# Optimization experiments

Hardware: AMD Instinct MI355X
Metric: run time of the kernel (lower is better)

The kernel has to match this reference:

```python
import jax, jax.numpy as jnp
import numpy as np
from jax import lax

SAMPLE_RATE = 44100.0


def _biquad(x, b0, b1, b2, a1, a2):
    """Direct-form-I biquad over last axis. x: [B,C,S]; coefs: [B,1] (broadcast over C).
    y[n] = b0*x[n] + b1*x[n-1] + b2*x[n-2] - a1*y[n-1] - a2*y[n-2], zero initial state
    (identical to torchaudio.functional.biquad)."""

    def step(carry, xn):  # xn: [B,C]
        x1, x2, y1, y2 = carry
        y = b0 * xn + b1 * x1 + b2 * x2 - a1 * y1 - a2 * y2
        return (xn, x1, y, y1), y

    xs = jnp.moveaxis(x, -1, 0)  # [S,B,C]
    z = jnp.zeros_like(x[..., 0])
    _, ys = lax.scan(step, (z, z, z, z), xs)
    return jnp.moveaxis(ys, 0, -1)  # [B,C,S]


def _peaking_coeffs(freq, gain, q):
    """RBJ peaking EQ coefficients, normalized by a0. Inputs: [B] -> outputs [B,1]."""
    w0 = 2.0 * jnp.pi * freq / SAMPLE_RATE
    alpha = jnp.sin(w0) / (2.0 * q)
    A = jnp.power(10.0, gain / 40.0)
    cosw0 = jnp.cos(w0)
    b0 = 1.0 + alpha * A
    b1 = -2.0 * cosw0
    b2 = 1.0 - alpha * A
    a0 = 1.0 + alpha / A
    a1 = -2.0 * cosw0
    a2 = 1.0 - alpha / A
    coefs = (b0 / a0, b1 / a0, b2 / a0, a1 / a0, a2 / a0)
    return tuple(c[:, None] for c in coefs)  # broadcast over channel dim


def setup_inputs() -> dict:
    key = jax.random.key(0)
    k1, k2, k3, k4 = jax.random.split(key, 4)
    B, C, S, NB = 32, 2, 262144, 10
    audio = jax.random.normal(k1, (B, C, S), dtype=jnp.float32)
    center_freqs = jax.random.uniform(k2, (B, NB), dtype=jnp.float32, minval=100.0, maxval=10000.0)
    gains = jax.random.uniform(k3, (B, NB), dtype=jnp.float32, minval=-12.0, maxval=12.0)
    q_factors = jax.random.uniform(k4, (B, NB), dtype=jnp.float32, minval=0.5, maxval=4.0)
    return {"audio": audio, "center_freqs": center_freqs, "gains": gains, "q_factors": q_factors}


def reference(audio, center_freqs, gains, q_factors):
    num_bands = center_freqs.shape[1]
    out = audio
    for band in range(num_bands):  # fixed small cascade of structurally distinct filters
        b0, b1, b2, a1, a2 = _peaking_coeffs(center_freqs[:, band], gains[:, band], q_factors[:, band])
        out = _biquad(out, b0, b1, b2, a1, a2)
    return out
```

## Files before the change

### kernel.cpp

```cpp
#include <hip/hip_runtime.h>


#define B_   32
#define C_   2
#define S_   262144
#define NB   10
#define SEQ  64

#define F_LCH   64
#define F_PCH   4096
#define F_G     8
#define F_GRP   512
#define F_NPOW  11

#define F_OFF_POW 1600
#define F_OFF_T   142400
#define F_OFF_G   5385280
#define F_OFF_SB  6040640
#define F_TOT     6696000

__global__ __launch_bounds__(256) void setup_kernel(
    const float* __restrict__ freqs, const float* __restrict__ gains,
    const float* __restrict__ qs, float* __restrict__ coef,
    float* __restrict__ powers) {
  __shared__ float bufA[400], bufB[400];
  __shared__ float cfs[NB * 5];
  const int b = blockIdx.x, tid = threadIdx.x;
  for (int e = tid; e < 400; e += 256) bufA[e] = 0.0f;
  if (tid < NB) {
    int idx = b * NB + tid;
    float f = freqs[idx], g = gains[idx], Q = qs[idx];
    float w0 = 6.28318530717958648f * f / 44100.0f;
    float sw = sinf(w0), cw = cosf(w0);
    float alpha = sw / (2.0f * Q);
    float A = expf(g * 0.05756462732485114f);
    float aA = alpha * A, adA = alpha / A;
    float inv = 1.0f / (1.0f + adA);
    float c0 = (1.0f + aA) * inv;
    float c1 = -2.0f * cw * inv;
    float c2 = (1.0f - aA) * inv;
    float c3 = 2.0f * cw * inv;
    float c4 = -(1.0f - adA) * inv;
    cfs[tid*5+0] = c0; cfs[tid*5+1] = c1; cfs[tid*5+2] = c2;
    cfs[tid*5+3] = c3; cfs[tid*5+4] = c4;
    float* o = coef + idx * 5;
    o[0] = c0; o[1] = c1; o[2] = c2; o[3] = c3; o[4] = c4;
  }
  __syncthreads();
  if (tid < 20) {
    int c = tid;
    float rp = 0.0f;
    for (int k = 0; k < NB; k++) {
      float b0 = cfs[k*5+0], b1 = cfs[k*5+1], b2 = cfs[k*5+2];
      float na1 = cfs[k*5+3], na2 = cfs[k*5+4];
      float val = (k > 0) ? b0 * rp : 0.0f;
      if (k > 0) {
        if (c == 2*k-2) val += b1;
        if (c == 2*k-1) val += b2;
      }
      if (c == 2*k)   val += na1;
      if (c == 2*k+1) val += na2;
      bufA[2*k*20 + c] = val;
      rp = val;
      if (c == 2*k) bufA[(2*k+1)*20 + c] = 1.0f;
    }
  }
  __syncthreads();
  float* cur = bufA;
  float* nxt = bufB;
  float* pw = powers + (size_t)b * F_NPOW * 400;
  for (int j = 1; j <= 17; j++) {
    for (int e = tid; e < 400; e += 256) {
      int r = e / 20, c = e % 20;
      float acc = 0.0f;
      #pragma unroll
      for (int k = 0; k < 20; k++) acc = fmaf(cur[r*20+k], cur[k*20+c], acc);
      nxt[e] = acc;
    }
    __syncthreads();
    { float* t_ = cur; cur = nxt; nxt = t_; }
    int slot = -1;
    if (j == 6) slot = 0;
    else if (j == 8) slot = 1;
    else if (j == 9) slot = 2;
    else if (j >= 10) slot = j - 7;
    if (slot >= 0) for (int e = tid; e < 400; e += 256) pw[slot*400 + e] = cur[e];
  }
}

template <bool WRITE_OUT>
__global__ __launch_bounds__(64) void pass_v3(
    const float* __restrict__ x, const float* __restrict__ coef,
    const float* __restrict__ tst, float* __restrict__ tout,
    float* __restrict__ out) {
  __shared__ float4 lds4[1024];
  const int seq = blockIdx.y;
  const int b = seq >> 1;
  const int lane = threadIdx.x;
  const int wgc0 = blockIdx.x * 64;
  const int chunk = wgc0 + lane;
  const float* cf = coef + b * NB * 5;
  float b0[NB], b1[NB], b2[NB], na1[NB], na2[NB];
  #pragma unroll
  for (int k = 0; k < NB; k++) {
    b0[k] = cf[k*5+0]; b1[k] = cf[k*5+1]; b2[k] = cf[k*5+2];
    na1[k] = cf[k*5+3]; na2[k] = cf[k*5+4];
  }
  const size_t span0 = (size_t)seq * S_ + (size_t)wgc0 * F_LCH;
  const float4* gx = (const float4*)(x + span0);
  #pragma unroll 4
  for (int it = 0; it < 16; it++) {
    int f = it * 64 + lane;
    float4 v = gx[f];
    int c = f >> 4, q = f & 15;
    lds4[c*16 + (q ^ (c & 15))] = v;
  }
  __syncthreads();
  float x1 = 0.0f, x2 = 0.0f;
  if (lane == 0) {
    if (chunk > 0) {
      const float* xs = x + span0;
      x1 = xs[-1]; x2 = xs[-2];
    }
  } else {
    float4 pv = lds4[(lane-1)*16 + (15 ^ ((lane-1) & 15))];
    x2 = pv.z; x1 = pv.w;
  }
  float p[NB], q_[NB];
  if (WRITE_OUT && chunk > 0) {
    const float4* sv = (const float4*)(tst + ((size_t)seq * F_PCH + chunk - 1) * 20);
    #pragma unroll
    for (int i = 0; i < 5; i++) {
      float4 a = sv[i];
      p[2*i] = a.x; q_[2*i] = a.y; p[2*i+1] = a.z; q_[2*i+1] = a.w;
    }
  } else {
    #pragma unroll
    for (int k = 0; k < NB; k++) { p[k] = 0.0f; q_[k] = 0.0f; }
  }
  #pragma unroll 2
  for (int qq = 0; qq < 16; qq++) {
    const int slot = lane*16 + (qq ^ (lane & 15));
    float4 xv = lds4[slot];
    float xin[4] = {xv.x, xv.y, xv.z, xv.w};
    float o[4];
    #pragma unroll
    for (int j = 0; j < 4; j++) {
      float u = xin[j], u1 = x1, u2 = x2;
      x2 = x1; x1 = xin[j];
      #pragma unroll
      for (int k = 0; k < NB; k++) {
        float v = fmaf(b0[k], u,
                  fmaf(b1[k], u1,
                  fmaf(b2[k], u2,
                  fmaf(na1[k], p[k], na2[k] * q_[k]))));
        u1 = p[k]; u2 = q_[k];
        q_[k] = p[k]; p[k] = v;
        u = v;
      }
      o[j] = u;
    }
    if (WRITE_OUT) lds4[slot] = make_float4(o[0], o[1], o[2], o[3]);
  }
  if (WRITE_OUT) {
    __syncthreads();
    float4* gy = (float4*)(out + span0);
    #pragma unroll 4
    for (int it = 0; it < 16; it++) {
      int f = it * 64 + lane;
      int c = f >> 4, q = f & 15;
      gy[f] = lds4[c*16 + (q ^ (c & 15))];
    }
  } else {
    float4* td = (float4*)(tout + ((size_t)seq * F_PCH + chunk) * 20);
    #pragma unroll
    for (int i = 0; i < 5; i++)
      td[i] = make_float4(p[2*i], q_[2*i], p[2*i+1], q_[2*i+1]);
  }
}

template <bool WRITE_BACK>
__global__ __launch_bounds__(256) void scan_horner(
    float* __restrict__ t, const float* __restrict__ powers,
    float* __restrict__ gbuf, const float* __restrict__ sbuf) {
  __shared__ float Msh[400];
  const int seq = blockIdx.y, b = seq >> 1;
  const int g = blockIdx.x * 256 + threadIdx.x;
  const float* pw0 = powers + (size_t)b * F_NPOW * 400;
  for (int e = threadIdx.x; e < 400; e += 256) {
    int r = e / 20, c = e % 20;
    Msh[c*20 + r] = pw0[e];
  }
  __syncthreads();
  float s[20];
  if (WRITE_BACK) {
    const float4* sv = (const float4*)(sbuf + ((size_t)seq * F_GRP + g) * 20);
    #pragma unroll
    for (int i = 0; i < 5; i++) {
      float4 a = sv[i];
      s[4*i] = a.x; s[4*i+1] = a.y; s[4*i+2] = a.z; s[4*i+3] = a.w;
    }
  } else {
    #pragma unroll
    for (int r = 0; r < 20; r++) s[r] = 0.0f;
  }
  float* tp = t + ((size_t)seq * F_PCH + (size_t)g * F_G) * 20;
  const float4* tv = (const float4*)tp;
  float4 nx[5];
  #pragma unroll
  for (int i = 0; i < 5; i++) nx[i] = tv[i];
  #pragma unroll 1
  for (int j = 0; j < F_G; j++) {
    float ns[20];
    #pragma unroll
    for (int i = 0; i < 5; i++) {
      float4 a = nx[i];
      ns[4*i] = a.x; ns[4*i+1] = a.y; ns[4*i+2] = a.z; ns[4*i+3] = a.w;
    }
    if (j < F_G - 1) {
      #pragma unroll
      for (int i = 0; i < 5; i++) nx[i] = tv[(j+1)*5 + i];
    }
    #pragma unroll
    for (int c = 0; c < 20; c++) {
      float vc = s[c];
      const float4* col = (const float4*)&Msh[c*20];
      float4 c0 = col[0], c1 = col[1], c2 = col[2], c3 = col[3], c4 = col[4];
      ns[0]  = fmaf(c0.x, vc, ns[0]);  ns[1]  = fmaf(c0.y, vc, ns[1]);
      ns[2]  = fmaf(c0.z, vc, ns[2]);  ns[3]  = fmaf(c0.w, vc, ns[3]);
      ns[4]  = fmaf(c1.x, vc, ns[4]);  ns[5]  = fmaf(c1.y, vc, ns[5]);
      ns[6]  = fmaf(c1.z, vc, ns[6]);  ns[7]  = fmaf(c1.w, vc, ns[7]);
      ns[8]  = fmaf(c2.x, vc, ns[8]);  ns[9]  = fmaf(c2.y, vc, ns[9]);
      ns[10] = fmaf(c2.z, vc, ns[10]); ns[11] = fmaf(c2.w, vc, ns[11]);
      ns[12] = fmaf(c3.x, vc, ns[12]); ns[13] = fmaf(c3.y, vc, ns[13]);
      ns[14] = fmaf(c3.z, vc, ns[14]); ns[15] = fmaf(c3.w, vc, ns[15]);
      ns[16] = fmaf(c4.x, vc, ns[16]); ns[17] = fmaf(c4.y, vc, ns[17]);
      ns[18] = fmaf(c4.z, vc, ns[18]); ns[19] = fmaf(c4.w, vc, ns[19]);
    }
    #pragma unroll
    for (int r = 0; r < 20; r++) s[r] = ns[r];
    if (WRITE_BACK) {
      float4* tw = (float4*)(tp + j * 20);
      #pragma unroll
      for (int i = 0; i < 5; i++)
        tw[i] = make_float4(s[4*i], s[4*i+1], s[4*i+2], s[4*i+3]);
    }
  }
  if (!WRITE_BACK) {
    float4* gw = (float4*)(gbuf + ((size_t)seq * F_GRP + g) * 20);
    #pragma unroll
    for (int i = 0; i < 5; i++)
      gw[i] = make_float4(s[4*i], s[4*i+1], s[4*i+2], s[4*i+3]);
  }
}

__global__ __launch_bounds__(512) void scan_ks(
    const float* __restrict__ gbuf, const float* __restrict__ powers,
    float* __restrict__ sbuf) {
  __shared__ float h[F_GRP * 20];
  __shared__ float Ksh[400];
  const int seq = blockIdx.x, b = seq >> 1, i = threadIdx.x;
  const float* pw = powers + (size_t)b * F_NPOW * 400;
  float own[20];
  {
    const float4* gv = (const float4*)(gbuf + ((size_t)seq * F_GRP + i) * 20);
    #pragma unroll
    for (int k = 0; k < 5; k++) {
      float4 a = gv[k];
      own[4*k] = a.x; own[4*k+1] = a.y; own[4*k+2] = a.z; own[4*k+3] = a.w;
    }
  }
  #pragma unroll
  for (int r = 0; r < 20; r++) h[i*20 + r] = own[r];
  for (int s = 0; s < 9; s++) {
    const int d = 1 << s;
    const float* pwS = pw + (size_t)(2 + s) * 400;
    __syncthreads();
    for (int e = i; e < 400; e += 512) {
      int r = e / 20, c = e % 20;
      Ksh[c*20 + r] = pwS[e];
    }
    float nb[20];
    if (i >= d) {
      const float4* hv = (const float4*)&h[(i - d) * 20];
      #pragma unroll
      for (int k = 0; k < 5; k++) {
        float4 a = hv[k];
        nb[4*k] = a.x; nb[4*k+1] = a.y; nb[4*k+2] = a.z; nb[4*k+3] = a.w;
      }
    }
    __syncthreads();
    if (i >= d) {
      #pragma unroll
      for (int c = 0; c < 20; c++) {
        float vc = nb[c];
        const float4* col = (const float4*)&Ksh[c*20];
        float4 c0 = col[0], c1 = col[1], c2 = col[2], c3 = col[3], c4 = col[4];
        own[0]  = fmaf(c0.x, vc, own[0]);  own[1]  = fmaf(c0.y, vc, own[1]);
        own[2]  = fmaf(c0.z, vc, own[2]);  own[3]  = fmaf(c0.w, vc, own[3]);
        own[4]  = fmaf(c1.x, vc, own[4]);  own[5]  = fmaf(c1.y, vc, own[5]);
        own[6]  = fmaf(c1.z, vc, own[6]);  own[7]  = fmaf(c1.w, vc, own[7]);
        own[8]  = fmaf(c2.x, vc, own[8]);  own[9]  = fmaf(c2.y, vc, own[9]);
        own[10] = fmaf(c2.z, vc, own[10]); own[11] = fmaf(c2.w, vc, own[11]);
        own[12] = fmaf(c3.x, vc, own[12]); own[13] = fmaf(c3.y, vc, own[13]);
        own[14] = fmaf(c3.z, vc, own[14]); own[15] = fmaf(c3.w, vc, own[15]);
        own[16] = fmaf(c4.x, vc, own[16]); own[17] = fmaf(c4.y, vc, own[17]);
        own[18] = fmaf(c4.z, vc, own[18]); own[19] = fmaf(c4.w, vc, own[19]);
      }
      #pragma unroll
      for (int r = 0; r < 20; r++) h[i*20 + r] = own[r];
    }
  }
  __syncthreads();
  float4* sw = (float4*)(sbuf + ((size_t)seq * F_GRP + i) * 20);
  if (i > 0) {
    const float4* hv = (const float4*)&h[(i - 1) * 20];
    #pragma unroll
    for (int k = 0; k < 5; k++) sw[k] = hv[k];
  } else {
    #pragma unroll
    for (int k = 0; k < 5; k++) sw[k] = make_float4(0.f, 0.f, 0.f, 0.f);
  }
}

extern "C" void kernel_launch(void* const* d_in, const int* in_sizes, int n_in,
                              void* d_out, int out_size, void* d_ws, size_t ws_size,
                              hipStream_t stream) {
  const float* audio = (const float*)d_in[0];
  const float* freqs = (const float*)d_in[1];
  const float* gains = (const float*)d_in[2];
  const float* qs    = (const float*)d_in[3];
  float* out = (float*)d_out;
  float* ws  = (float*)d_ws;
  float* coef   = ws;
  float* powers = ws + F_OFF_POW;
  float* t      = ws + F_OFF_T;
  float* gbuf   = ws + F_OFF_G;
  float* sbuf   = ws + F_OFF_SB;

  hipLaunchKernelGGL(setup_kernel, dim3(B_), dim3(256), 0, stream,
                     freqs, gains, qs, coef, powers);
  hipLaunchKernelGGL((pass_v3<false>), dim3(F_PCH / 64, SEQ), dim3(64), 0, stream,
                     audio, coef, (const float*)nullptr, t, (float*)nullptr);
  hipLaunchKernelGGL((scan_horner<false>), dim3(F_GRP / 256, SEQ), dim3(256),
                     0, stream, t, powers, gbuf, (const float*)nullptr);
  hipLaunchKernelGGL(scan_ks, dim3(SEQ), dim3(512), 0, stream,
                     gbuf, powers, sbuf);
  hipLaunchKernelGGL((scan_horner<true>), dim3(F_GRP / 256, SEQ), dim3(256),
                     0, stream, t, powers, (float*)nullptr, sbuf);
  hipLaunchKernelGGL((pass_v3<true>), dim3(F_PCH / 64, SEQ), dim3(64), 0, stream,
                     audio, coef, t, (float*)nullptr, out);
}
```

Measured before the change: 236.1 us.

## Fuse three scan stages into one kernel and exploit block-triangular transition matrices

Merges the two Horner scan passes and the Kogge-Stone scan into a single per-sequence kernel that keeps group states in shared memory, removing two launches and the gbuf/sbuf round trips through global memory. It exploits the block lower-triangular structure of the cascade's state-transition matrix to skip roughly half the FMAs, both in the matrix-power setup and in the matrix-vector updates. Powers are now stored pre-transposed, and shared-memory rows are rotated to avoid bank conflicts. The zero-state pass now loads each chunk straight into registers and gets neighbouring samples by wave shuffle instead of staging through LDS. The fused scan runs only 64 blocks, which limits parallelism in that stage, and the in-kernel loads of the matrix from global memory could add latency.

Measured after the change: 266.7 us. 1.13x slower.

```diff
diff --git a/kernel.cpp b/kernel.cpp
--- a/kernel.cpp
+++ b/kernel.cpp
@@ -2,27 +2,35 @@
 
 
 #define B_   32
-#define C_   2
 #define S_   262144
 #define NB   10
 #define SEQ  64
-
-#define F_LCH   64
-#define F_PCH   4096
-#define F_G     8
-#define F_GRP   512
-#define F_NPOW  11
-
-#define F_OFF_POW 1600
-#define F_OFF_T   142400
-#define F_OFF_G   5385280
-#define F_OFF_SB  6040640
-#define F_TOT     6696000
+#define LCH  64
+#define PCH  4096
+#define GG   8
+#define GRP  512
+#define NPOW 10
+
+#define WS_POW 1600
+#define WS_T   129600
+
+__device__ __forceinline__ void trimv_acc(float* __restrict__ acc,
+                                          const float* __restrict__ M,
+                                          const float* __restrict__ v) {
+  #pragma unroll
+  for (int c = 0; c < 20; ++c) {
+    const int rlo = c & ~1;
+    const float vc = v[c];
+    #pragma unroll
+    for (int r = rlo; r < 20; ++r)
+      acc[r] = fmaf(M[c * 20 + r], vc, acc[r]);
+  }
+}
 
 __global__ __launch_bounds__(256) void setup_kernel(
     const float* __restrict__ freqs, const float* __restrict__ gains,
     const float* __restrict__ qs, float* __restrict__ coef,
-    float* __restrict__ powers) {
+    float* __restrict__ powT) {
   __shared__ float bufA[400], bufB[400];
   __shared__ float cfs[NB * 5];
   const int b = blockIdx.x, tid = threadIdx.x;
@@ -68,37 +76,39 @@
   __syncthreads();
   float* cur = bufA;
   float* nxt = bufB;
-  float* pw = powers + (size_t)b * F_NPOW * 400;
+  float* pw = powT + (size_t)b * NPOW * 400;
   for (int j = 1; j <= 17; j++) {
     for (int e = tid; e < 400; e += 256) {
       int r = e / 20, c = e % 20;
       float acc = 0.0f;
-      #pragma unroll
-      for (int k = 0; k < 20; k++) acc = fmaf(cur[r*20+k], cur[k*20+c], acc);
+      if ((c >> 1) <= (r >> 1)) {
+        const int klo = c & ~1, khi = r | 1;
+        for (int k = klo; k <= khi; ++k)
+          acc = fmaf(cur[r*20+k], cur[k*20+c], acc);
+      }
       nxt[e] = acc;
     }
     __syncthreads();
     { float* t_ = cur; cur = nxt; nxt = t_; }
     int slot = -1;
     if (j == 6) slot = 0;
-    else if (j == 8) slot = 1;
-    else if (j == 9) slot = 2;
-    else if (j >= 10) slot = j - 7;
-    if (slot >= 0) for (int e = tid; e < 400; e += 256) pw[slot*400 + e] = cur[e];
-  }
-}
-
-template <bool WRITE_OUT>
-__global__ __launch_bounds__(64) void pass_v3(
+    else if (j >= 9) slot = j - 8;
+    if (slot >= 0) {
+      for (int e = tid; e < 400; e += 256) {
+        int r = e / 20, c = e % 20;
+        if ((c >> 1) <= (r >> 1))
+          pw[slot*400 + c*20 + r] = cur[r*20+c];
+      }
+    }
+  }
+}
+
+__global__ __launch_bounds__(256) void pass_zero(
     const float* __restrict__ x, const float* __restrict__ coef,
-    const float* __restrict__ tst, float* __restrict__ tout,
-    float* __restrict__ out) {
-  __shared__ float4 lds4[1024];
-  const int seq = blockIdx.y;
-  const int b = seq >> 1;
-  const int lane = threadIdx.x;
-  const int wgc0 = blockIdx.x * 64;
-  const int chunk = wgc0 + lane;
+    float* __restrict__ t) {
+  const int seq = blockIdx.y, b = seq >> 1;
+  const int chunk = blockIdx.x * 256 + threadIdx.x;
+  const int lane = threadIdx.x & 63;
   const float* cf = coef + b * NB * 5;
   float b0[NB], b1[NB], b2[NB], na1[NB], na2[NB];
   #pragma unroll
@@ -106,44 +116,24 @@
     b0[k] = cf[k*5+0]; b1[k] = cf[k*5+1]; b2[k] = cf[k*5+2];
     na1[k] = cf[k*5+3]; na2[k] = cf[k*5+4];
   }
-  const size_t span0 = (size_t)seq * S_ + (size_t)wgc0 * F_LCH;
-  const float4* gx = (const float4*)(x + span0);
-  #pragma unroll 4
-  for (int it = 0; it < 16; it++) {
-    int f = it * 64 + lane;
-    float4 v = gx[f];
-    int c = f >> 4, q = f & 15;
-    lds4[c*16 + (q ^ (c & 15))] = v;
-  }
-  __syncthreads();
-  float x1 = 0.0f, x2 = 0.0f;
+  const float* xs = x + (size_t)seq * S_ + (size_t)chunk * LCH;
+  const float4* xv = (const float4*)xs;
+  float4 xr[16];
+  #pragma unroll
+  for (int i = 0; i < 16; i++) xr[i] = xv[i];
+  float up_z = __shfl_up(xr[15].z, 1, 64);
+  float up_w = __shfl_up(xr[15].w, 1, 64);
+  float x1, x2;
   if (lane == 0) {
-    if (chunk > 0) {
-      const float* xs = x + span0;
-      x1 = xs[-1]; x2 = xs[-2];
-    }
-  } else {
-    float4 pv = lds4[(lane-1)*16 + (15 ^ ((lane-1) & 15))];
-    x2 = pv.z; x1 = pv.w;
-  }
+    x1 = 0.0f; x2 = 0.0f;
+    if (chunk > 0) { x1 = xs[-1]; x2 = xs[-2]; }
+  } else { x1 = up_w; x2 = up_z; }
   float p[NB], q_[NB];
-  if (WRITE_OUT && chunk > 0) {
-    const float4* sv = (const float4*)(tst + ((size_t)seq * F_PCH + chunk - 1) * 20);
-    #pragma unroll
-    for (int i = 0; i < 5; i++) {
-      float4 a = sv[i];
-      p[2*i] = a.x; q_[2*i] = a.y; p[2*i+1] = a.z; q_[2*i+1] = a.w;
-    }
-  } else {
-    #pragma unroll
-    for (int k = 0; k < NB; k++) { p[k] = 0.0f; q_[k] = 0.0f; }
-  }
-  #pragma unroll 2
+  #pragma unroll
+  for (int k = 0; k < NB; k++) { p[k] = 0.0f; q_[k] = 0.0f; }
+  #pragma unroll
   for (int qq = 0; qq < 16; qq++) {
-    const int slot = lane*16 + (qq ^ (lane & 15));
-    float4 xv = lds4[slot];
-    float xin[4] = {xv.x, xv.y, xv.z, xv.w};
-    float o[4];
+    float xin[4] = {xr[qq].x, xr[qq].y, xr[qq].z, xr[qq].w};
     #pragma unroll
     for (int j = 0; j < 4; j++) {
       float u = xin[j], u1 = x1, u2 = x2;
@@ -158,168 +148,163 @@
         q_[k] = p[k]; p[k] = v;
         u = v;
       }
-      o[j] = u;
-    }
-    if (WRITE_OUT) lds4[slot] = make_float4(o[0], o[1], o[2], o[3]);
-  }
-  if (WRITE_OUT) {
+    }
+  }
+  float4* td = (float4*)(t + ((size_t)seq * PCH + chunk) * 20);
+  #pragma unroll
+  for (int i = 0; i < 5; i++)
+    td[i] = make_float4(p[2*i], q_[2*i], p[2*i+1], q_[2*i+1]);
+}
+
+__device__ __forceinline__ void h_write(float4* __restrict__ h4, int j,
+                                        const float* __restrict__ s) {
+  const int m5 = j % 5;
+  #pragma unroll
+  for (int k = 0; k < 5; k++) {
+    int sl = k + m5; if (sl >= 5) sl -= 5;
+    h4[j*5 + sl] = make_float4(s[4*k], s[4*k+1], s[4*k+2], s[4*k+3]);
+  }
+}
+__device__ __forceinline__ void h_read(const float4* __restrict__ h4, int j,
+                                       float* __restrict__ s) {
+  const int m5 = j % 5;
+  #pragma unroll
+  for (int k = 0; k < 5; k++) {
+    int sl = k + m5; if (sl >= 5) sl -= 5;
+    float4 a = h4[j*5 + sl];
+    s[4*k] = a.x; s[4*k+1] = a.y; s[4*k+2] = a.z; s[4*k+3] = a.w;
+  }
+}
+
+__global__ __launch_bounds__(512) void scan_kernel(
+    float* __restrict__ t, const float* __restrict__ powT) {
+  __shared__ float4 h4[GRP * 5];
+  const int seq = blockIdx.x, b = seq >> 1, i = threadIdx.x;
+  const float* M = powT + (size_t)b * NPOW * 400;
+  float* tb = t + (size_t)seq * PCH * 20;
+  float s[20];
+  #pragma unroll
+  for (int r = 0; r < 20; r++) s[r] = 0.0f;
+  for (int j = 0; j < GG; j++) {
+    float ns[20];
+    const float4* tv = (const float4*)(tb + ((size_t)i * GG + j) * 20);
+    #pragma unroll
+    for (int k = 0; k < 5; k++) {
+      float4 a = tv[k];
+      ns[4*k] = a.x; ns[4*k+1] = a.y; ns[4*k+2] = a.z; ns[4*k+3] = a.w;
+    }
+    trimv_acc(ns, M, s);
+    #pragma unroll
+    for (int r = 0; r < 20; r++) s[r] = ns[r];
+  }
+  h_write(h4, i, s);
+  for (int st = 0; st < 9; st++) {
+    const int d = 1 << st;
+    const float* K = M + (size_t)(1 + st) * 400;
     __syncthreads();
-    float4* gy = (float4*)(out + span0);
-    #pragma unroll 4
-    for (int it = 0; it < 16; it++) {
-      int f = it * 64 + lane;
-      int c = f >> 4, q = f & 15;
-      gy[f] = lds4[c*16 + (q ^ (c & 15))];
-    }
+    float nb[20];
+    const bool en = (i >= d);
+    if (en) h_read(h4, i - d, nb);
+    __syncthreads();
+    if (en) {
+      trimv_acc(s, K, nb);
+      h_write(h4, i, s);
+    }
+  }
+  __syncthreads();
+  float P[20];
+  if (i > 0) {
+    h_read(h4, i - 1, P);
   } else {
-    float4* td = (float4*)(tout + ((size_t)seq * F_PCH + chunk) * 20);
-    #pragma unroll
-    for (int i = 0; i < 5; i++)
-      td[i] = make_float4(p[2*i], q_[2*i], p[2*i+1], q_[2*i+1]);
-  }
-}
-
-template <bool WRITE_BACK>
-__global__ __launch_bounds__(256) void scan_horner(
-    float* __restrict__ t, const float* __restrict__ powers,
-    float* __restrict__ gbuf, const float* __restrict__ sbuf) {
-  __shared__ float Msh[400];
+    for (int r = 0; r < 20; r++) P[r] = 0.0f;
+  }
+  for (int j = 0; j < GG; j++) {
+    float ns[20];
+    float* tp = tb + ((size_t)i * GG + j) * 20;
+    const float4* tv = (const float4*)tp;
+    #pragma unroll
+    for (int k = 0; k < 5; k++) {
+      float4 a = tv[k];
+      ns[4*k] = a.x; ns[4*k+1] = a.y; ns[4*k+2] = a.z; ns[4*k+3] = a.w;
+    }
+    trimv_acc(ns, M, P);
+    #pragma unroll
+    for (int r = 0; r < 20; r++) P[r] = ns[r];
+    float4* tw = (float4*)tp;
+    #pragma unroll
+    for (int k = 0; k < 5; k++)
+      tw[k] = make_float4(P[4*k], P[4*k+1], P[4*k+2], P[4*k+3]);
+  }
+}
+
+__global__ __launch_bounds__(64) void pass_out(
+    const float* __restrict__ x, const float* __restrict__ coef,
+    const float* __restrict__ t, float* __restrict__ out) {
+  __shared__ float4 lds4[1024];
   const int seq = blockIdx.y, b = seq >> 1;
-  const int g = blockIdx.x * 256 + threadIdx.x;
-  const float* pw0 = powers + (size_t)b * F_NPOW * 400;
-  for (int e = threadIdx.x; e < 400; e += 256) {
-    int r = e / 20, c = e % 20;
-    Msh[c*20 + r] = pw0[e];
-  }
-  __syncthreads();
-  float s[20];
-  if (WRITE_BACK) {
-    const float4* sv = (const float4*)(sbuf + ((size_t)seq * F_GRP + g) * 20);
+  const int lane = threadIdx.x;
+  const int chunk = blockIdx.x * 64 + lane;
+  const float* cf = coef + b * NB * 5;
+  float b0[NB], b1[NB], b2[NB], na1[NB], na2[NB];
+  #pragma unroll
+  for (int k = 0; k < NB; k++) {
+    b0[k] = cf[k*5+0]; b1[k] = cf[k*5+1]; b2[k] = cf[k*5+2];
+    na1[k] = cf[k*5+3]; na2[k] = cf[k*5+4];
+  }
+  const size_t span0 = (size_t)seq * S_ + (size_t)blockIdx.x * 64 * LCH;
+  const float* xs = x + (size_t)seq * S_ + (size_t)chunk * LCH;
+  const float4* xv = (const float4*)xs;
+  float4 xr[16];
+  #pragma unroll
+  for (int i = 0; i < 16; i++) xr[i] = xv[i];
+  float up_z = __shfl_up(xr[15].z, 1, 64);
+  float up_w = __shfl_up(xr[15].w, 1, 64);
+  float x1, x2;
+  if (lane == 0) {
+    x1 = 0.0f; x2 = 0.0f;
+    if (chunk > 0) { x1 = xs[-1]; x2 = xs[-2]; }
+  } else { x1 = up_w; x2 = up_z; }
+  float p[NB], q_[NB];
+  if (chunk > 0) {
+    const float4* sv = (const float4*)(t + ((size_t)seq * PCH + chunk - 1) * 20);
     #pragma unroll
     for (int i = 0; i < 5; i++) {
       float4 a = sv[i];
-      s[4*i] = a.x; s[4*i+1] = a.y; s[4*i+2] = a.z; s[4*i+3] = a.w;
+      p[2*i] = a.x; q_[2*i] = a.y; p[2*i+1] = a.z; q_[2*i+1] = a.w;
     }
   } else {
     #pragma unroll
-    for (int r = 0; r < 20; r++) s[r] = 0.0f;
-  }
-  float* tp = t + ((size_t)seq * F_PCH + (size_t)g * F_G) * 20;
-  const float4* tv = (const float4*)tp;
-  float4 nx[5];
-  #pragma unroll
-  for (int i = 0; i < 5; i++) nx[i] = tv[i];
-  #pragma unroll 1
-  for (int j = 0; j < F_G; j++) {
-    float ns[20];
-    #pragma unroll
-    for (int i = 0; i < 5; i++) {
-      float4 a = nx[i];
-      ns[4*i] = a.x; ns[4*i+1] = a.y; ns[4*i+2] = a.z; ns[4*i+3] = a.w;
-    }
-    if (j < F_G - 1) {
+    for (int k = 0; k < NB; k++) { p[k] = 0.0f; q_[k] = 0.0f; }
+  }
+  #pragma unroll
+  for (int qq = 0; qq < 16; qq++) {
+    float xin[4] = {xr[qq].x, xr[qq].y, xr[qq].z, xr[qq].w};
+    float o[4];
+    #pragma unroll
+    for (int j = 0; j < 4; j++) {
+      float u = xin[j], u1 = x1, u2 = x2;
+      x2 = x1; x1 = xin[j];
       #pragma unroll
-      for (int i = 0; i < 5; i++) nx[i] = tv[(j+1)*5 + i];
-    }
-    #pragma unroll
-    for (int c = 0; c < 20; c++) {
-      float vc = s[c];
-      const float4* col = (const float4*)&Msh[c*20];
-      float4 c0 = col[0], c1 = col[1], c2 = col[2], c3 = col[3], c4 = col[4];
-      ns[0]  = fmaf(c0.x, vc, ns[0]);  ns[1]  = fmaf(c0.y, vc, ns[1]);
-      ns[2]  = fmaf(c0.z, vc, ns[2]);  ns[3]  = fmaf(c0.w, vc, ns[3]);
-      ns[4]  = fmaf(c1.x, vc, ns[4]);  ns[5]  = fmaf(c1.y, vc, ns[5]);
-      ns[6]  = fmaf(c1.z, vc, ns[6]);  ns[7]  = fmaf(c1.w, vc, ns[7]);
-      ns[8]  = fmaf(c2.x, vc, ns[8]);  ns[9]  = fmaf(c2.y, vc, ns[9]);
-      ns[10] = fmaf(c2.z, vc, ns[10]); ns[11] = fmaf(c2.w, vc, ns[11]);
-      ns[12] = fmaf(c3.x, vc, ns[12]); ns[13] = fmaf(c3.y, vc, ns[13]);
-      ns[14] = fmaf(c3.z, vc, ns[14]); ns[15] = fmaf(c3.w, vc, ns[15]);
-      ns[16] = fmaf(c4.x, vc, ns[16]); ns[17] = fmaf(c4.y, vc, ns[17]);
-      ns[18] = fmaf(c4.z, vc, ns[18]); ns[19] = fmaf(c4.w, vc, ns[19]);
-    }
-    #pragma unroll
-    for (int r = 0; r < 20; r++) s[r] = ns[r];
-    if (WRITE_BACK) {
-      float4* tw = (float4*)(tp + j * 20);
-      #pragma unroll
-      for (int i = 0; i < 5; i++)
-        tw[i] = make_float4(s[4*i], s[4*i+1], s[4*i+2], s[4*i+3]);
-    }
-  }
-  if (!WRITE_BACK) {
-    float4* gw = (float4*)(gbuf + ((size_t)seq * F_GRP + g) * 20);
-    #pragma unroll
-    for (int i = 0; i < 5; i++)
-      gw[i] = make_float4(s[4*i], s[4*i+1], s[4*i+2], s[4*i+3]);
-  }
-}
-
-__global__ __launch_bounds__(512) void scan_ks(
-    const float* __restrict__ gbuf, const float* __restrict__ powers,
-    float* __restrict__ sbuf) {
-  __shared__ float h[F_GRP * 20];
-  __shared__ float Ksh[400];
-  const int seq = blockIdx.x, b = seq >> 1, i = threadIdx.x;
-  const float* pw = powers + (size_t)b * F_NPOW * 400;
-  float own[20];
-  {
-    const float4* gv = (const float4*)(gbuf + ((size_t)seq * F_GRP + i) * 20);
-    #pragma unroll
-    for (int k = 0; k < 5; k++) {
-      float4 a = gv[k];
-      own[4*k] = a.x; own[4*k+1] = a.y; own[4*k+2] = a.z; own[4*k+3] = a.w;
-    }
-  }
-  #pragma unroll
-  for (int r = 0; r < 20; r++) h[i*20 + r] = own[r];
-  for (int s = 0; s < 9; s++) {
-    const int d = 1 << s;
-    const float* pwS = pw + (size_t)(2 + s) * 400;
-    __syncthreads();
-    for (int e = i; e < 400; e += 512) {
-      int r = e / 20, c = e % 20;
-      Ksh[c*20 + r] = pwS[e];
-    }
-    float nb[20];
-    if (i >= d) {
-      const float4* hv = (const float4*)&h[(i - d) * 20];
-      #pragma unroll
-      for (int k = 0; k < 5; k++) {
-        float4 a = hv[k];
-        nb[4*k] = a.x; nb[4*k+1] = a.y; nb[4*k+2] = a.z; nb[4*k+3] = a.w;
-      }
-    }
-    __syncthreads();
-    if (i >= d) {
-      #pragma unroll
-      for (int c = 0; c < 20; c++) {
-        float vc = nb[c];
-        const float4* col = (const float4*)&Ksh[c*20];
-        float4 c0 = col[0], c1 = col[1], c2 = col[2], c3 = col[3], c4 = col[4];
-        own[0]  = fmaf(c0.x, vc, own[0]);  own[1]  = fmaf(c0.y, vc, own[1]);
-        own[2]  = fmaf(c0.z, vc, own[2]);  own[3]  = fmaf(c0.w, vc, own[3]);
-        own[4]  = fmaf(c1.x, vc, own[4]);  own[5]  = fmaf(c1.y, vc, own[5]);
-        own[6]  = fmaf(c1.z, vc, own[6]);  own[7]  = fmaf(c1.w, vc, own[7]);
-        own[8]  = fmaf(c2.x, vc, own[8]);  own[9]  = fmaf(c2.y, vc, own[9]);
-        own[10] = fmaf(c2.z, vc, own[10]); own[11] = fmaf(c2.w, vc, own[11]);
-        own[12] = fmaf(c3.x, vc, own[12]); own[13] = fmaf(c3.y, vc, own[13]);
-        own[14] = fmaf(c3.z, vc, own[14]); own[15] = fmaf(c3.w, vc, own[15]);
-        own[16] = fmaf(c4.x, vc, own[16]); own[17] = fmaf(c4.y, vc, own[17]);
-        own[18] = fmaf(c4.z, vc, own[18]); own[19] = fmaf(c4.w, vc, own[19]);
-      }
-      #pragma unroll
-      for (int r = 0; r < 20; r++) h[i*20 + r] = own[r];
-    }
+      for (int k = 0; k < NB; k++) {
+        float v = fmaf(b0[k], u,
+                  fmaf(b1[k], u1,
+                  fmaf(b2[k], u2,
+                  fmaf(na1[k], p[k], na2[k] * q_[k]))));
+        u1 = p[k]; u2 = q_[k];
+        q_[k] = p[k]; p[k] = v;
+        u = v;
+      }
+      o[j] = u;
+    }
+    lds4[lane*16 + (qq ^ (lane & 15))] = make_float4(o[0], o[1], o[2], o[3]);
   }
   __syncthreads();
-  float4* sw = (float4*)(sbuf + ((size_t)seq * F_GRP + i) * 20);
-  if (i > 0) {
-    const float4* hv = (const float4*)&h[(i - 1) * 20];
-    #pragma unroll
-    for (int k = 0; k < 5; k++) sw[k] = hv[k];
-  } else {
-    #pragma unroll
-    for (int k = 0; k < 5; k++) sw[k] = make_float4(0.f, 0.f, 0.f, 0.f);
+  float4* gy = (float4*)(out + span0);
+  #pragma unroll 4
+  for (int it = 0; it < 16; it++) {
+    int f = it * 64 + lane;
+    int c = f >> 4, q = f & 15;
+    gy[f] = lds4[c*16 + (q ^ (c & 15))];
   }
 }
 
@@ -330,24 +315,17 @@
   const float* freqs = (const float*)d_in[1];
   const float* gains = (const float*)d_in[2];
   const float* qs    = (const float*)d_in[3];
-  float* out = (float*)d_out;
-  float* ws  = (float*)d_ws;
-  float* coef   = ws;
-  float* powers = ws + F_OFF_POW;
-  float* t      = ws + F_OFF_T;
-  float* gbuf   = ws + F_OFF_G;
-  float* sbuf   = ws + F_OFF_SB;
+  float* out  = (float*)d_out;
+  float* ws   = (float*)d_ws;
+  float* coef = ws;
+  float* powT = ws + WS_POW;
+  float* t    = ws + WS_T;
 
   hipLaunchKernelGGL(setup_kernel, dim3(B_), dim3(256), 0, stream,
-                     freqs, gains, qs, coef, powers);
-  hipLaunchKernelGGL((pass_v3<false>), dim3(F_PCH / 64, SEQ), dim3(64), 0, stream,
-                     audio, coef, (const float*)nullptr, t, (float*)nullptr);
-  hipLaunchKernelGGL((scan_horner<false>), dim3(F_GRP / 256, SEQ), dim3(256),
-                     0, stream, t, powers, gbuf, (const float*)nullptr);
-  hipLaunchKernelGGL(scan_ks, dim3(SEQ), dim3(512), 0, stream,
-                     gbuf, powers, sbuf);
-  hipLaunchKernelGGL((scan_horner<true>), dim3(F_GRP / 256, SEQ), dim3(256),
-                     0, stream, t, powers, (float*)nullptr, sbuf);
-  hipLaunchKernelGGL((pass_v3<true>), dim3(F_PCH / 64, SEQ), dim3(64), 0, stream,
-                     audio, coef, t, (float*)nullptr, out);
-}
+                     freqs, gains, qs, coef, powT);
+  hipLaunchKernelGGL(pass_zero, dim3(PCH / 256, SEQ), dim3(256), 0, stream,
+                     audio, coef, t);
+  hipLaunchKernelGGL(scan_kernel, dim3(SEQ), dim3(512), 0, stream, t, powT);
+  hipLaunchKernelGGL(pass_out, dim3(PCH / 64, SEQ), dim3(64), 0, stream,
+                     audio, coef, t, out);
+}
```
